# Performance work log

Hardware: AMD Instinct MI355X
Metric: run time of the kernel (lower is better)

Reference implementation:

```python
import jax, jax.numpy as jnp
import numpy as np

# module hyperparameters (match init_kwargs)
IN_PLANES = 64
OUT = 64            # out_planes
N_HASHES = 4
CHUNK = 25          # chunk_size
GROUPS = 8
KS = 56             # kernel_size == attended axis length H
GP = OUT // GROUPS  # group_planes = 8
EPS_N = 5e-5        # F.normalize eps
BN_EPS = 1e-5
F_GW, F_GV1, F_GV2 = 0.1, 0.1, 1.0


def l2norm(x, axis):
    # torch F.normalize(p=2, eps=EPS_N)
    n = jnp.sqrt(jnp.sum(x * x, axis=axis, keepdims=True))
    return x / jnp.maximum(n, EPS_N)


def setup_inputs() -> dict:
    key = jax.random.key(0)
    k1, k2, k3, k4 = jax.random.split(key, 4)
    x = jax.random.normal(k1, (2, IN_PLANES, KS, 56), jnp.float32)
    conv_w = jax.random.normal(k2, (OUT * 3 // 2, IN_PLANES), jnp.float32) * np.float32(np.sqrt(1.0 / IN_PLANES))
    bn_gamma = jnp.ones((OUT * 3 // 2,), jnp.float32)
    bn_beta = jnp.zeros((OUT * 3 // 2,), jnp.float32)
    relative = jax.random.normal(k3, (KS, GP * 3 // 2), jnp.float32) * np.float32(np.sqrt(1.0 / GP))
    # LSH random rotations: hash_buckets = min(56//25 + (56//25)%2, 10) = 2 -> hb//2 = 1
    rotations = jax.random.normal(k4, (OUT // 2, N_HASHES, 1), jnp.float32)
    return dict(x=x, conv_w=conv_w, bn_gamma=bn_gamma, bn_beta=bn_beta,
                relative=relative, rotations=rotations)


def reference(x, conv_w, bn_gamma, bn_beta, relative, rotations):
    # width=False: (N,C,H,W) -> (N,W,C,H), flatten batch with W
    N, C, Hax, W = x.shape
    x = jnp.transpose(x, (0, 3, 1, 2)).reshape(N * W, C, Hax)
    B, H = N * W, Hax
    hash_buckets = min(H // CHUNK + (H // CHUNK) % 2, 10)

    # 1x1 conv + eval-mode BatchNorm (running_mean=0, running_var=1)
    qkv = jnp.einsum('oc,bch->boh', conv_w, x)
    qkv = qkv / np.float32(np.sqrt(1.0 + BN_EPS)) * bn_gamma[None, :, None] + bn_beta[None, :, None]
    # NOTE: original uses raw reshape (B,C3,H) -> (B,H,C3), NOT a transpose
    qkv = qkv.reshape(B, H, OUT * 3 // 2)
    w_match = qkv[..., :OUT // 2]   # (B,H,out/2)
    v_match = qkv[..., OUT // 2:]   # (B,H,out)
    w_emb = relative[:, :GP // 2]
    v_emb = relative[:, GP // 2:]

    # LSH hashing (rotations shared across batch)
    rot = jnp.einsum('btf,fhi->bhti', w_match, rotations)
    rot = jnp.concatenate([rot, -rot], axis=-1)           # (B,nh,H,hash_buckets)
    codes = jnp.argmax(rot, axis=-1)
    codes = codes + (jnp.arange(N_HASHES) * hash_buckets)[None, :, None]
    codes = codes.reshape(B, N_HASHES * H)

    indices = jnp.argsort(codes, axis=-1)                 # stable sort into buckets
    undo = jnp.argsort(indices, axis=-1)
    mod = indices % H
    w_s = jnp.take_along_axis(w_match, mod[:, :, None], axis=1)
    v_s = jnp.take_along_axis(v_match, mod[:, :, None], axis=1)

    padding = (CHUNK - H % CHUNK) % CHUNK                 # 19 here
    w_b = w_s.reshape(B, N_HASHES, H, OUT // 2)
    v_b = v_s.reshape(B, N_HASHES, H, OUT)
    if padding:
        w_b = jnp.concatenate([w_b, w_b[:, :, -padding:, :]], axis=2)
        v_b = jnp.concatenate([v_b, v_b[:, :, -padding:, :]], axis=2)
        w_emb = jnp.concatenate([w_emb, w_emb[-padding:, :]], axis=0)
        v_emb = jnp.concatenate([v_emb, v_emb[-padding:, :]], axis=0)
    # raw reshapes, exactly as torch does (groups folded via flat reshape)
    w_b = w_b.reshape(B, GROUPS, N_HASHES, -1, CHUNK, GP // 2)
    v_b = v_b.reshape(B, GROUPS, N_HASHES, -1, CHUNK, GP)
    w_emb = w_emb.reshape(-1, CHUNK, GP // 2)             # (K,25,4)
    v_emb = v_emb.reshape(-1, CHUNK, GP)                  # (K,25,8)
    K = w_emb.shape[0]

    def adj(t):  # look-around over the chunk axis (dim 3), cat on dim 4
        return jnp.concatenate([t, jnp.roll(t, 1, axis=3), jnp.roll(t, -1, axis=3)], axis=4)

    def adj_emb(t):
        return jnp.concatenate([t, jnp.roll(t, 1, axis=0), jnp.roll(t, -1, axis=0)], axis=1)

    w_m = adj(l2norm(w_b, -1))
    v_a = adj(v_b)
    w_e = adj_emb(w_emb)
    v_e = adj_emb(v_emb)

    raw = jnp.einsum('bghkie,bghkje->bghkij', w_b, w_m)            # (B,g,h,K,25,75)
    emb_sc = F_GW * jnp.einsum('bghkie,kje->bghkij', w_b, w_e)
    ss = jnp.concatenate([raw, emb_sc], axis=1)                    # (B,2g,h,K,25,75)
    ss = l2norm(ss, 1).reshape(B, 2, GROUPS, N_HASHES, K, CHUNK, CHUNK * 3).sum(axis=1)

    bs = jax.nn.logsumexp(ss, axis=-1, keepdims=True)
    score = jnp.exp(ss - bs)
    bs = bs.reshape(B, GROUPS, N_HASHES, K * CHUNK)

    r_out = F_GV2 * jnp.einsum('bgukij,bgukje->bgukie', score, v_a)
    r_emb = F_GV1 * jnp.einsum('bgukij,kje->bgukie', score, v_e)
    ret = jnp.concatenate([r_out, r_emb], axis=-1)                 # (B,g,h,K,25,2*gp)
    ret = ret.reshape(B, N_HASHES, K, CHUNK, OUT * 2)              # raw reshape
    ret = ret.reshape(B, OUT * 2, N_HASHES, K, CHUNK)              # raw reshape
    ret = l2norm(ret, 1).reshape(B, N_HASHES, K, CHUNK, OUT, 2).sum(axis=-1)
    bs = l2norm(bs, 1).sum(axis=1)                                 # (B,h,K*25)

    ret = ret.reshape(B, N_HASHES, K * CHUNK, OUT)
    if padding:
        ret = ret[:, :, :-padding, :]
        bs = bs[:, :, :-padding]
    ret = ret.reshape(B, N_HASHES * H, OUT)
    bs = bs.reshape(B, N_HASHES * H)

    ret = jnp.take_along_axis(ret, undo[:, :, None], axis=1)      # unsort
    bs = jnp.take_along_axis(bs, undo, axis=1)
    ret = ret.reshape(B, N_HASHES, H, OUT)
    bs = bs.reshape(B, N_HASHES, H, 1)

    probs = jax.nn.softmax(bs, axis=1)
    ret = jnp.sum(ret * probs, axis=1)                             # (B,H,out)
    ret = ret.reshape(N, W, H, OUT)
    return jnp.transpose(ret, (0, 3, 2, 1))                        # (N,out,H,W)
```

## Files before the change

kernel.cpp:

```cpp
#include <hip/hip_runtime.h>
#include <math.h>


#define EPSN 5e-5f
#define INV_EPSN 20000.0f
#define LOG2E 1.4426950408889634f
#define LN2   0.6931471805599453f

__device__ __forceinline__ float dot4(const float4 a, const float4 b) {
    return a.x * b.x + a.y * b.y + a.z * b.z + a.w * b.w;
}
__device__ __forceinline__ void fma4(float4& a, float s, const float4 v) {
    a.x += s * v.x; a.y += s * v.y; a.z += s * v.z; a.w += s * v.w;
}

__global__ __launch_bounds__(256) void k12_qkv_sort(
        const float* __restrict__ x, const float* __restrict__ cw,
        const float* __restrict__ gamma, const float* __restrict__ beta,
        const float* __restrict__ rot, float* __restrict__ qkv,
        int* __restrict__ idx_buf) {
    __shared__ float xsT[56 * 68];
    __shared__ float cws[96 * 64];
    __shared__ float wm[56 * 32];
    __shared__ float rl[128];
    __shared__ float gs[96], bt[96];
    __shared__ int code[224];
    __shared__ int srt[224];
    const int b = blockIdx.x, n = b / 56, w = b % 56, tid = threadIdx.x;
    const float* xb = x + n * 200704 + w;
    #pragma unroll 7
    for (int i = tid; i < 3584; i += 256) {
        int c = i / 56, h = i % 56;
        xsT[h * 68 + c] = xb[c * 3136 + h * 56];
    }
    #pragma unroll 8
    for (int i = tid; i < 6144; i += 256) cws[i] = cw[i];
    if (tid < 128) rl[tid] = rot[tid];
    if (tid < 96) { gs[tid] = gamma[tid]; bt[tid] = beta[tid]; }
    __syncthreads();
    const float inv_s = 1.0f / sqrtf(1.0f + 1.0e-5f);
    for (int tl = tid; tl < 1344; tl += 256) {
        int oq = tl / 56, h = tl % 56;
        int o0 = oq * 4;
        float s0 = 0.f, s1 = 0.f, s2 = 0.f, s3 = 0.f;
        #pragma unroll
        for (int cs = 0; cs < 16; ++cs) {
            float4 xv = *(const float4*)&xsT[h * 68 + cs * 4];
            float4 c0 = *(const float4*)&cws[(o0 + 0) * 64 + cs * 4];
            float4 c1 = *(const float4*)&cws[(o0 + 1) * 64 + cs * 4];
            float4 c2 = *(const float4*)&cws[(o0 + 2) * 64 + cs * 4];
            float4 c3 = *(const float4*)&cws[(o0 + 3) * 64 + cs * 4];
            s0 += dot4(xv, c0); s1 += dot4(xv, c1);
            s2 += dot4(xv, c2); s3 += dot4(xv, c3);
        }
        #pragma unroll
        for (int qq = 0; qq < 4; ++qq) {
            int o = o0 + qq;
            float sv = (qq == 0) ? s0 : (qq == 1) ? s1 : (qq == 2) ? s2 : s3;
            float val = sv * inv_s * gs[o] + bt[o];
            int j = o * 56 + h;
            qkv[b * 5376 + j] = val;
            int f = j % 96;
            if (f < 32) wm[(j / 96) * 32 + f] = val;
        }
    }
    __syncthreads();
    if (tid < 224) {
        int u = tid / 56, t = tid % 56;
        float s = 0.f;
        #pragma unroll 8
        for (int f = 0; f < 32; ++f) s += wm[t * 32 + f] * rl[f * 4 + u];
        code[tid] = ((s < 0.f) ? 1 : 0) + 2 * u;
    }
    __syncthreads();
    if (tid < 224) {
        int c = code[tid], r = 0;
        #pragma unroll 8
        for (int p = 0; p < 224; ++p) {
            int cp = code[p];
            r += (int)((cp < c) | ((cp == c) & (p < tid)));
        }
        srt[r] = tid;
    }
    __syncthreads();
    if (tid < 224) idx_buf[b * 224 + tid] = srt[tid];
}

__global__ __launch_bounds__(256) void k3_attn(
        const float* __restrict__ qkv, const int* __restrict__ idx_buf,
        const float* __restrict__ rel, float* __restrict__ Rb,
        float* __restrict__ bsb) {
    __shared__ __align__(16) float Wc[8][3][25][4];
    __shared__ __align__(16) float Vb[8][3][25][8];
    const int b = blockIdx.x, u = blockIdx.y, k = blockIdx.z;
    const int tid = threadIdx.x;
    const float* q = qkv + b * 5376;
    const int* ib = idx_buf + b * 224;

    #pragma unroll 3
    for (int idx = tid; idx < 600; idx += 256) {
        int i = idx % 25, kk = (idx / 25) % 3, g = idx / 75;
        int p0 = 1200 * g + 300 * u + 100 * kk + 4 * i;
        int h = p0 / 2400, r = p0 % 2400, t = r >> 5, f = r & 31;
        int row = (t < 56) ? t : t - 19;
        int tt = ib[h * 56 + row] % 56;
        float4 v = *(const float4*)&q[tt * 96 + f];
        float ni = fminf(__builtin_amdgcn_rsqf(dot4(v, v)), INV_EPSN);
        v.x *= ni; v.y *= ni; v.z *= ni; v.w *= ni;
        *(float4*)&Wc[g][kk][i][0] = v;
    }
    #pragma unroll 5
    for (int idx = tid; idx < 1200; idx += 256) {
        int half = idx & 1, fr = idx >> 1;
        int i = fr % 25, kk = (fr / 25) % 3, g = fr / 75;
        int p0 = 2400 * g + 600 * u + 200 * kk + 8 * i + 4 * half;
        int h = p0 / 4800, r = p0 % 4800, t = r >> 6, f = r & 63;
        int row = (t < 56) ? t : t - 19;
        int tt = ib[h * 56 + row] % 56;
        *(float4*)&Vb[g][kk][i][4 * half] = *(const float4*)&q[tt * 96 + 32 + f];
    }
    const int g = tid & 7, i = tid >> 3;
    float4 wbr = {0.f, 0.f, 0.f, 0.f};
    if (tid < 200) {
        int p0 = 1200 * g + 300 * u + 100 * k + 4 * i;
        int h = p0 / 2400, r = p0 % 2400, t = r >> 5, f = r & 31;
        int row = (t < 56) ? t : t - 19;
        int tt = ib[h * 56 + row] % 56;
        wbr = *(const float4*)&q[tt * 96 + f];
    }
    __syncthreads();
    if (tid < 200) {
        float se = 0.f;
        float4 a0 = {0,0,0,0}, a1 = {0,0,0,0}, a2 = {0,0,0,0}, a3 = {0,0,0,0};
        #pragma unroll
        for (int ks = 0; ks < 3; ++ks) {
            #pragma unroll
            for (int jj = 0; jj < 25; ++jj) {
                const int tw = ks * 25 + jj;
                const int roww = (tw < 56) ? tw : tw - 19;
                float4 we = *(const float4*)&rel[roww * 12];
                float rawv = dot4(wbr, *(const float4*)&Wc[g][ks][jj][0]);
                float embv = 0.1f * dot4(wbr, we);
                float p2 = rawv * rawv + embv * embv;
                p2 += __shfl_xor(p2, 1);
                p2 += __shfl_xor(p2, 2);
                p2 += __shfl_xor(p2, 4);
                float di = fminf(__builtin_amdgcn_rsqf(p2), INV_EPSN);
                float e = __builtin_amdgcn_exp2f((rawv + embv) * di * LOG2E);
                se += e;
                const float4* vv = (const float4*)&Vb[g][ks][jj][0];
                fma4(a0, e, vv[0]); fma4(a1, e, vv[1]);
                float4 ve0 = *(const float4*)&rel[roww * 12 + 4];
                float4 ve1 = *(const float4*)&rel[roww * 12 + 8];
                fma4(a2, e, ve0); fma4(a3, e, ve1);
            }
        }
        bsb[b * 2400 + g * 300 + u * 75 + k * 25 + i] =
            __builtin_amdgcn_logf(se) * LN2;
        const float rinv = 1.0f / se;
        const float r2 = 0.1f * rinv;
        a0.x *= rinv; a0.y *= rinv; a0.z *= rinv; a0.w *= rinv;
        a1.x *= rinv; a1.y *= rinv; a1.z *= rinv; a1.w *= rinv;
        a2.x *= r2;   a2.y *= r2;   a2.z *= r2;   a2.w *= r2;
        a3.x *= r2;   a3.y *= r2;   a3.z *= r2;   a3.w *= r2;
        float* rp = Rb + b * 38400 + 4800 * g + 1200 * u + 400 * k + 16 * i;
        ((float4*)rp)[0] = a0;
        ((float4*)rp)[1] = a1;
        ((float4*)rp)[2] = a2;
        ((float4*)rp)[3] = a3;
    }
}

__global__ __launch_bounds__(256) void k45_post(
        const float* __restrict__ Rb, const float* __restrict__ bsb,
        const int* __restrict__ idx_buf, float* __restrict__ out) {
    __shared__ float D[300];
    __shared__ float bsn[300];
    __shared__ float retU[224][64];
    __shared__ float bsU[224];
    __shared__ int idxL[224];
    const int b = blockIdx.x, tid = threadIdx.x;
    const int n = b / 56, w = b % 56;
    const float* R = Rb + b * 38400;
    if (tid < 224) idxL[tid] = idx_buf[b * 224 + tid];
    for (int r = tid; r < 300; r += 256) {
        float s = 0.f;
        #pragma unroll 16
        for (int c = 0; c < 128; ++c) { float v = R[c * 300 + r]; s += v * v; }
        D[r] = fminf(__builtin_amdgcn_rsqf(s), INV_EPSN);
    }
    for (int idx = tid; idx < 300; idx += 256) {
        int u = idx / 75, t = idx % 75;
        float s2 = 0.f, sum = 0.f;
        #pragma unroll
        for (int g = 0; g < 8; ++g) {
            float v = bsb[b * 2400 + g * 300 + u * 75 + t];
            s2 += v * v; sum += v;
        }
        bsn[idx] = sum / fmaxf(sqrtf(s2), EPSN);
    }
    __syncthreads();
    #pragma unroll 4
    for (int idx = tid; idx < 224 * 64; idx += 256) {
        int p = idx >> 6, o = idx & 63;
        int u3 = p / 56, t = p % 56;
        int k3 = t / 25, i3 = t % 25;
        int q0 = 9600 * u3 + 3200 * k3 + 128 * i3 + 2 * o;
        float2 rv = *(const float2*)&R[q0];
        int r0 = q0 % 300;
        float val = rv.x * D[r0] + rv.y * D[r0 + 1];
        int r = idxL[p];
        retU[r][o] = val;
        if (o == 0) bsU[r] = bsn[u3 * 75 + t];
    }
    __syncthreads();
    for (int idx = tid; idx < 56 * 64; idx += 256) {
        int h = idx >> 6, o = idx & 63;
        float b0 = bsU[h], b1 = bsU[56 + h], b2 = bsU[112 + h], b3 = bsU[168 + h];
        float m = fmaxf(fmaxf(b0, b1), fmaxf(b2, b3));
        float e0 = __builtin_amdgcn_exp2f((b0 - m) * LOG2E);
        float e1 = __builtin_amdgcn_exp2f((b1 - m) * LOG2E);
        float e2 = __builtin_amdgcn_exp2f((b2 - m) * LOG2E);
        float e3 = __builtin_amdgcn_exp2f((b3 - m) * LOG2E);
        float ps = e0 + e1 + e2 + e3;
        float val = (retU[h][o] * e0 + retU[56 + h][o] * e1 +
                     retU[112 + h][o] * e2 + retU[168 + h][o] * e3) / ps;
        out[((n * 64 + o) * 56 + h) * 56 + w] = val;
    }
}

extern "C" void kernel_launch(void* const* d_in, const int* in_sizes, int n_in,
                              void* d_out, int out_size, void* d_ws, size_t ws_size,
                              hipStream_t stream) {
    (void)in_sizes; (void)n_in; (void)out_size; (void)ws_size;
    const float* x     = (const float*)d_in[0];
    const float* cw    = (const float*)d_in[1];
    const float* gamma = (const float*)d_in[2];
    const float* beta  = (const float*)d_in[3];
    const float* rel   = (const float*)d_in[4];
    const float* rot   = (const float*)d_in[5];
    float* ws  = (float*)d_ws;
    float* qkv = ws;
    float* bsb = ws + 602112;
    float* Rb  = ws + 870912;
    int*   idx = (int*)(ws + 5171712);

    k12_qkv_sort<<<112, 256, 0, stream>>>(x, cw, gamma, beta, rot, qkv, idx);
    k3_attn<<<dim3(112, 4, 3), 256, 0, stream>>>(qkv, idx, rel, Rb, bsb);
    k45_post<<<112, 256, 0, stream>>>(Rb, bsb, idx, (float*)d_out);
}
```

Before: 174.1 us.

## Precompute attention norm table in LDS and split post kernel over output halves

The attention kernel now caches the sort indices and the query rows in LDS. It computes the per-(j,i) normalization denominators across groups once into a shared table, which removes the per-iteration cross-lane shuffles and rsqrt work. The relative embedding is folded into the key vectors so each inner step needs a single dot product. The post kernel is split across two blocks per batch row, each handling half of the output channels, to double parallelism and halve LDS use, at the cost of recomputing the norm and bs reductions in both blocks.

```diff
diff --git a/kernel.cpp b/kernel.cpp
--- a/kernel.cpp
+++ b/kernel.cpp
@@ -92,10 +92,15 @@
         float* __restrict__ bsb) {
     __shared__ __align__(16) float Wc[8][3][25][4];
     __shared__ __align__(16) float Vb[8][3][25][8];
+    __shared__ __align__(16) float WbK[8][25][4];
+    __shared__ float DIT[75][25];
+    __shared__ int ibL[224];
     const int b = blockIdx.x, u = blockIdx.y, k = blockIdx.z;
     const int tid = threadIdx.x;
     const float* q = qkv + b * 5376;
-    const int* ib = idx_buf + b * 224;
+
+    if (tid < 224) ibL[tid] = idx_buf[b * 224 + tid];
+    __syncthreads();
 
     #pragma unroll 3
     for (int idx = tid; idx < 600; idx += 256) {
@@ -103,8 +108,9 @@
         int p0 = 1200 * g + 300 * u + 100 * kk + 4 * i;
         int h = p0 / 2400, r = p0 % 2400, t = r >> 5, f = r & 31;
         int row = (t < 56) ? t : t - 19;
-        int tt = ib[h * 56 + row] % 56;
+        int tt = ibL[h * 56 + row] % 56;
         float4 v = *(const float4*)&q[tt * 96 + f];
+        if (kk == k) *(float4*)&WbK[g][i][0] = v;
         float ni = fminf(__builtin_amdgcn_rsqf(dot4(v, v)), INV_EPSN);
         v.x *= ni; v.y *= ni; v.z *= ni; v.w *= ni;
         *(float4*)&Wc[g][kk][i][0] = v;
@@ -116,37 +122,65 @@
         int p0 = 2400 * g + 600 * u + 200 * kk + 8 * i + 4 * half;
         int h = p0 / 4800, r = p0 % 4800, t = r >> 6, f = r & 63;
         int row = (t < 56) ? t : t - 19;
-        int tt = ib[h * 56 + row] % 56;
+        int tt = ibL[h * 56 + row] % 56;
         *(float4*)&Vb[g][kk][i][4 * half] = *(const float4*)&q[tt * 96 + 32 + f];
     }
-    const int g = tid & 7, i = tid >> 3;
-    float4 wbr = {0.f, 0.f, 0.f, 0.f};
+    __syncthreads();
+
+    if (tid < 250) {
+        const int i = tid % 25, jg = tid / 25;
+        float4 wb8[8];
+        #pragma unroll
+        for (int g = 0; g < 8; ++g) wb8[g] = *(const float4*)&WbK[g][i][0];
+        #pragma unroll
+        for (int it = 0; it < 8; ++it) {
+            int j = jg * 8 + it;
+            if (j < 75) {
+                int ks = j / 25, jj = j % 25;
+                int roww = (j < 56) ? j : j - 19;
+                float4 we = *(const float4*)&rel[roww * 12];
+                we.x *= 0.1f; we.y *= 0.1f; we.z *= 0.1f; we.w *= 0.1f;
+                float s2 = 0.f;
+                #pragma unroll
+                for (int g = 0; g < 8; ++g) {
+                    float4 wcn = *(const float4*)&Wc[g][ks][jj][0];
+                    float raw = dot4(wb8[g], wcn);
+                    float emb = dot4(wb8[g], we);
+                    s2 += raw * raw + emb * emb;
+                }
+                DIT[j][i] = fminf(__builtin_amdgcn_rsqf(s2), INV_EPSN);
+            }
+        }
+    }
+    __syncthreads();
+
+    #pragma unroll 3
+    for (int idx = tid; idx < 600; idx += 256) {
+        int i = idx % 25, kk = (idx / 25) % 3, g = idx / 75;
+        int tw = kk * 25 + i;
+        int roww = (tw < 56) ? tw : tw - 19;
+        float4 we = *(const float4*)&rel[roww * 12];
+        float4 v = *(const float4*)&Wc[g][kk][i][0];
+        v.x += 0.1f * we.x; v.y += 0.1f * we.y;
+        v.z += 0.1f * we.z; v.w += 0.1f * we.w;
+        *(float4*)&Wc[g][kk][i][0] = v;
+    }
+    __syncthreads();
+
     if (tid < 200) {
-        int p0 = 1200 * g + 300 * u + 100 * k + 4 * i;
-        int h = p0 / 2400, r = p0 % 2400, t = r >> 5, f = r & 31;
-        int row = (t < 56) ? t : t - 19;
-        int tt = ib[h * 56 + row] % 56;
-        wbr = *(const float4*)&q[tt * 96 + f];
-    }
-    __syncthreads();
-    if (tid < 200) {
+        const int g = tid & 7, i = tid >> 3;
+        const float4 wbr = *(const float4*)&WbK[g][i][0];
         float se = 0.f;
         float4 a0 = {0,0,0,0}, a1 = {0,0,0,0}, a2 = {0,0,0,0}, a3 = {0,0,0,0};
         #pragma unroll
         for (int ks = 0; ks < 3; ++ks) {
             #pragma unroll
             for (int jj = 0; jj < 25; ++jj) {
-                const int tw = ks * 25 + jj;
-                const int roww = (tw < 56) ? tw : tw - 19;
-                float4 we = *(const float4*)&rel[roww * 12];
-                float rawv = dot4(wbr, *(const float4*)&Wc[g][ks][jj][0]);
-                float embv = 0.1f * dot4(wbr, we);
-                float p2 = rawv * rawv + embv * embv;
-                p2 += __shfl_xor(p2, 1);
-                p2 += __shfl_xor(p2, 2);
-                p2 += __shfl_xor(p2, 4);
-                float di = fminf(__builtin_amdgcn_rsqf(p2), INV_EPSN);
-                float e = __builtin_amdgcn_exp2f((rawv + embv) * di * LOG2E);
+                const int jP = ks * 25 + jj;
+                const int roww = (jP < 56) ? jP : jP - 19;
+                float di = DIT[jP][i];
+                float e = __builtin_amdgcn_exp2f(
+                    dot4(wbr, *(const float4*)&Wc[g][ks][jj][0]) * di * LOG2E);
                 se += e;
                 const float4* vv = (const float4*)&Vb[g][ks][jj][0];
                 fma4(a0, e, vv[0]); fma4(a1, e, vv[1]);
@@ -176,11 +210,11 @@
         const int* __restrict__ idx_buf, float* __restrict__ out) {
     __shared__ float D[300];
     __shared__ float bsn[300];
-    __shared__ float retU[224][64];
+    __shared__ float retU[224][32];
     __shared__ float bsU[224];
     __shared__ int idxL[224];
-    const int b = blockIdx.x, tid = threadIdx.x;
-    const int n = b / 56, w = b % 56;
+    const int b = blockIdx.x, oh = blockIdx.y, tid = threadIdx.x;
+    const int n = b / 56, w = b % 56, o0 = oh * 32;
     const float* R = Rb + b * 38400;
     if (tid < 224) idxL[tid] = idx_buf[b * 224 + tid];
     for (int r = tid; r < 300; r += 256) {
@@ -200,22 +234,26 @@
         bsn[idx] = sum / fmaxf(sqrtf(s2), EPSN);
     }
     __syncthreads();
+    if (tid < 224) {
+        int u3 = tid / 56, t = tid % 56;
+        bsU[idxL[tid]] = bsn[u3 * 75 + t];
+    }
     #pragma unroll 4
-    for (int idx = tid; idx < 224 * 64; idx += 256) {
-        int p = idx >> 6, o = idx & 63;
+    for (int idx = tid; idx < 224 * 32; idx += 256) {
+        int p = idx >> 5, oc = idx & 31;
+        int o = o0 + oc;
         int u3 = p / 56, t = p % 56;
         int k3 = t / 25, i3 = t % 25;
         int q0 = 9600 * u3 + 3200 * k3 + 128 * i3 + 2 * o;
         float2 rv = *(const float2*)&R[q0];
         int r0 = q0 % 300;
         float val = rv.x * D[r0] + rv.y * D[r0 + 1];
-        int r = idxL[p];
-        retU[r][o] = val;
-        if (o == 0) bsU[r] = bsn[u3 * 75 + t];
-    }
-    __syncthreads();
-    for (int idx = tid; idx < 56 * 64; idx += 256) {
-        int h = idx >> 6, o = idx & 63;
+        retU[idxL[p]][oc] = val;
+    }
+    __syncthreads();
+    for (int idx = tid; idx < 56 * 32; idx += 256) {
+        int h = idx >> 5, oc = idx & 31;
+        int o = o0 + oc;
         float b0 = bsU[h], b1 = bsU[56 + h], b2 = bsU[112 + h], b3 = bsU[168 + h];
         float m = fmaxf(fmaxf(b0, b1), fmaxf(b2, b3));
         float e0 = __builtin_amdgcn_exp2f((b0 - m) * LOG2E);
@@ -223,8 +261,8 @@
         float e2 = __builtin_amdgcn_exp2f((b2 - m) * LOG2E);
         float e3 = __builtin_amdgcn_exp2f((b3 - m) * LOG2E);
         float ps = e0 + e1 + e2 + e3;
-        float val = (retU[h][o] * e0 + retU[56 + h][o] * e1 +
-                     retU[112 + h][o] * e2 + retU[168 + h][o] * e3) / ps;
+        float val = (retU[h][oc] * e0 + retU[56 + h][oc] * e1 +
+                     retU[112 + h][oc] * e2 + retU[168 + h][oc] * e3) / ps;
         out[((n * 64 + o) * 56 + h) * 56 + w] = val;
     }
 }
@@ -247,5 +285,5 @@
 
     k12_qkv_sort<<<112, 256, 0, stream>>>(x, cw, gamma, beta, rot, qkv, idx);
     k3_attn<<<dim3(112, 4, 3), 256, 0, stream>>>(qkv, idx, rel, Rb, bsb);
-    k45_post<<<112, 256, 0, stream>>>(Rb, bsb, idx, (float*)d_out);
-}
+    k45_post<<<dim3(112, 2), 256, 0, stream>>>(Rb, bsb, idx, (float*)d_out);
+}
```

Measured after the change: 154.5 us. 1.13x faster.
